# Kernel tuning notes

Hardware: AMD Instinct MI355X
Metric: run time of the kernel (lower is better)

The kernel has to match this reference:

```python
import jax, jax.numpy as jnp
import numpy as np

N_NODES = 50000
N_EDGES = 800000
D = 64
B = 64
HL = 128  # lstm hidden
OUT = 32


def setup_inputs() -> dict:
    key = jax.random.key(0)
    ks = jax.random.split(key, 16)
    s = 0.05
    return {
        "x": jax.random.normal(ks[0], (N_NODES, D), jnp.float32),
        "edge_index": jax.random.randint(ks[1], (2, N_EDGES), 0, N_NODES),
        "batch": jnp.sort(jax.random.randint(ks[2], (N_NODES,), 0, B)),
        "w1": jax.random.normal(ks[3], (D, D), jnp.float32) * s,
        "b1": jnp.zeros((D,), jnp.float32),
        "w2": jax.random.normal(ks[4], (D, D), jnp.float32) * s,
        "b2": jnp.zeros((D,), jnp.float32),
        "w3": jax.random.normal(ks[5], (D, D), jnp.float32) * s,
        "b3": jnp.zeros((D,), jnp.float32),
        "w4": jax.random.normal(ks[6], (D, D), jnp.float32) * s,
        "b4": jnp.zeros((D,), jnp.float32),
        "w_ih": jax.random.normal(ks[7], (4 * HL, D), jnp.float32) * s,
        "w_hh": jax.random.normal(ks[8], (4 * HL, HL), jnp.float32) * s,
        "b_ih": jnp.zeros((4 * HL,), jnp.float32),
        "b_hh": jnp.zeros((4 * HL,), jnp.float32),
        "fc_w": jax.random.normal(ks[9], (OUT, HL), jnp.float32) * s,
        "fc_b": jnp.zeros((OUT,), jnp.float32),
        "h0": jax.random.normal(ks[10], (1, B, HL), jnp.float32),
        "c0": jax.random.normal(ks[11], (1, B, HL), jnp.float32),
    }


def _gin(x, edge_index, wA, bA, wB, bB):
    # GINConv with eps=0: MLP(x + sum_{j->i} x_j); scatter-add over edges
    agg = jax.ops.segment_sum(x[edge_index[0]], edge_index[1], num_segments=N_NODES)
    h = x + agg
    h = jax.nn.relu(h @ wA.T + bA)
    return h @ wB.T + bB


def reference(x, edge_index, batch, w1, b1, w2, b2, w3, b3, w4, b4,
              w_ih, w_hh, b_ih, b_hh, fc_w, fc_b, h0, c0):
    h = jax.nn.relu(_gin(x, edge_index, w1, b1, w2, b2))  # dropout = identity (eval)
    h = jax.nn.relu(_gin(h, edge_index, w3, b3, w4, b4))
    # global_mean_pool over graphs
    sums = jax.ops.segment_sum(h, batch, num_segments=B)              # [B, D]
    cnts = jax.ops.segment_sum(jnp.ones((N_NODES,), h.dtype), batch, num_segments=B)
    pooled = sums / jnp.maximum(cnts, 1.0)[:, None]
    # single-step LSTM (PyTorch gate order: i, f, g, o)
    gates = pooled @ w_ih.T + b_ih + h0[0] @ w_hh.T + b_hh            # [B, 4H]
    i, f, g, o = jnp.split(gates, 4, axis=-1)
    c1 = jax.nn.sigmoid(f) * c0[0] + jax.nn.sigmoid(i) * jnp.tanh(g)
    h1 = jax.nn.sigmoid(o) * jnp.tanh(c1)
    logits = h1 @ fc_w.T + fc_b
    probs = jax.nn.softmax(logits, axis=1)
    return probs, h1[None], c1[None]
```

## Files before the change

kernel.cpp:

```cpp
#include <hip/hip_runtime.h>
#include <hip/hip_bf16.h>

#define N_NODES 50000
#define N_EDGES 800000
#define D 64
#define B 64
#define HL 128
#define OUT 32

#define CAP 64
#define STP 72
#define PK 8
#define ZROW N_NODES

#define BINS 196
#define EPB 2048
#define LCAP 48
#define BCAP 4608

typedef __attribute__((ext_vector_type(8))) short          short8;
typedef __attribute__((ext_vector_type(8))) unsigned short ushort8_t;
typedef __attribute__((ext_vector_type(4))) float          floatx4;

__device__ __forceinline__ unsigned short f2bf(float f)
{
    unsigned u = __float_as_uint(f);
    u = (u + 0x7FFFu + ((u >> 16) & 1u)) >> 16;
    return (unsigned short)u;
}
__device__ __forceinline__ float bf2f(unsigned short s)
{
    return __uint_as_float(((unsigned)s) << 16);
}

__global__ __launch_bounds__(256) void cvt_kernel(
    const float* __restrict__ x, unsigned short* __restrict__ xb,
    const float* __restrict__ w1, const float* __restrict__ w2,
    const float* __restrict__ w3, const float* __restrict__ w4,
    unsigned short* __restrict__ wb,
    int* __restrict__ bincnt,
    unsigned short* __restrict__ g, unsigned short* __restrict__ h1)
{
    int i = blockIdx.x * 256 + threadIdx.x;
    const float4 v = reinterpret_cast<const float4*>(x)[i];
    ushort4 o;
    o.x = f2bf(v.x); o.y = f2bf(v.y); o.z = f2bf(v.z); o.w = f2bf(v.w);
    reinterpret_cast<ushort4*>(xb)[i] = o;

    if (blockIdx.x < 64) {
        int j = blockIdx.x * 256 + threadIdx.x;
        int m = j >> 12, off = j & 4095;
        const float* src = (m == 0) ? w1 : (m == 1) ? w2 : (m == 2) ? w3 : w4;
        wb[j] = f2bf(src[off]);
    }

    if (blockIdx.x == 64) {
        int t = threadIdx.x;
        bincnt[t] = 0;
        if (t < D) {
            xb[(size_t)ZROW * D + t] = 0;
            g [(size_t)ZROW * D + t] = 0;
            h1[(size_t)ZROW * D + t] = 0;
        }
    }
}

__global__ __launch_bounds__(256) void binA_kernel(
    const int* __restrict__ ei, int* __restrict__ bincnt,
    unsigned* __restrict__ binbuf)
{
    __shared__ int      lcnt[BINS];
    __shared__ int      gbase[BINS];
    __shared__ unsigned lbuf[BINS * LCAP];

    int t = threadIdx.x;
    if (t < BINS) lcnt[t] = 0;
    __syncthreads();

    int base = blockIdx.x * EPB;
#pragma unroll
    for (int i = 0; i < EPB / 256; ++i) {
        int e = base + i * 256 + t;
        if (e < N_EDGES) {
            int s = ei[e];
            int d = ei[N_EDGES + e];
            int bin = d >> 8;
            unsigned pk = (unsigned)s | ((unsigned)(d & 255) << 16);
            int p = atomicAdd(&lcnt[bin], 1);
            if (p < LCAP) {
                lbuf[bin * LCAP + p] = pk;
            } else {
                int q = atomicAdd(&bincnt[bin], 1);
                if (q < BCAP) binbuf[bin * BCAP + q] = pk;
            }
        }
    }
    __syncthreads();

    if (t < BINS) {
        int m = lcnt[t]; m = (m < LCAP) ? m : LCAP;
        gbase[t] = (m > 0) ? atomicAdd(&bincnt[t], m) : 0;
    }
    __syncthreads();

    int wv = t >> 6, lane = t & 63;
    for (int b = wv; b < BINS; b += 4) {
        int m = lcnt[b]; m = (m < LCAP) ? m : LCAP;
        int gb = gbase[b];
        for (int j = lane; j < m; j += 64)
            if (gb + j < BCAP) binbuf[b * BCAP + gb + j] = lbuf[b * LCAP + j];
    }
}

__global__ __launch_bounds__(256) void binB_kernel(
    const int*      __restrict__ bincnt,
    const unsigned* __restrict__ binbuf,
    int*            __restrict__ cnt,
    unsigned short* __restrict__ bucket)
{
    __shared__ int            lc[256];
    __shared__ unsigned short lbkt[256 * CAP];

    int t = threadIdx.x;
    lc[t] = 0;
    {
        ushort8_t fill = {ZROW, ZROW, ZROW, ZROW, ZROW, ZROW, ZROW, ZROW};
        for (int idx = t; idx < 256 * CAP / 8; idx += 256)
            reinterpret_cast<ushort8_t*>(lbkt)[idx] = fill;
    }
    __syncthreads();

    int bin = blockIdx.x;
    int m = bincnt[bin]; m = (m < BCAP) ? m : BCAP;
    const unsigned* src = binbuf + bin * BCAP;
    for (int j = t; j < m; j += 256) {
        unsigned pk = src[j];
        int dlow = (pk >> 16) & 255;
        int p = atomicAdd(&lc[dlow], 1);
        if (p < CAP) lbkt[dlow * CAP + p] = (unsigned short)(pk & 0xFFFFu);
    }
    __syncthreads();

    int n0 = bin * 256;
    int n = n0 + t;
    if (n < N_NODES) cnt[n] = (lc[t] < CAP) ? lc[t] : CAP;

    for (int idx = t; idx < 256 * 8; idx += 256) {
        int r = idx >> 3, c = idx & 7;
        if (n0 + r < N_NODES)
            *reinterpret_cast<ushort8_t*>(
                bucket + (size_t)(n0 + r) * CAP + c * 8) =
                *reinterpret_cast<const ushort8_t*>(&lbkt[r * CAP + c * 8]);
    }
}

__global__ __launch_bounds__(256) void gather_kernel(
    const unsigned short* __restrict__ feat,
    const int*            __restrict__ cnt,
    const unsigned short* __restrict__ bucket,
    unsigned short*       __restrict__ outp)
{
    int wv = threadIdx.x >> 6, lane = threadIdx.x & 63;
    int n = blockIdx.x * 4 + wv;

    int deg = cnt[n];
    deg = (deg < CAP) ? deg : CAP;
    int rounds = (deg + 15) >> 4;
    const unsigned short* bkt = bucket + (size_t)n * CAP;

    float acc = bf2f(feat[(size_t)n * D + lane]);
    for (int r = 0; r < rounds; ++r) {
        ushort8_t ia = *reinterpret_cast<const ushort8_t*>(bkt + r * 16);
        ushort8_t ib = *reinterpret_cast<const ushort8_t*>(bkt + r * 16 + 8);
        float v0 = bf2f(feat[(size_t)ia[0] * D + lane]);
        float v1 = bf2f(feat[(size_t)ia[1] * D + lane]);
        float v2 = bf2f(feat[(size_t)ia[2] * D + lane]);
        float v3 = bf2f(feat[(size_t)ia[3] * D + lane]);
        float v4 = bf2f(feat[(size_t)ia[4] * D + lane]);
        float v5 = bf2f(feat[(size_t)ia[5] * D + lane]);
        float v6 = bf2f(feat[(size_t)ia[6] * D + lane]);
        float v7 = bf2f(feat[(size_t)ia[7] * D + lane]);
        float v8 = bf2f(feat[(size_t)ib[0] * D + lane]);
        float v9 = bf2f(feat[(size_t)ib[1] * D + lane]);
        float va = bf2f(feat[(size_t)ib[2] * D + lane]);
        float vb = bf2f(feat[(size_t)ib[3] * D + lane]);
        float vc = bf2f(feat[(size_t)ib[4] * D + lane]);
        float vd = bf2f(feat[(size_t)ib[5] * D + lane]);
        float ve = bf2f(feat[(size_t)ib[6] * D + lane]);
        float vf = bf2f(feat[(size_t)ib[7] * D + lane]);
        acc += (((v0 + v1) + (v2 + v3)) + ((v4 + v5) + (v6 + v7)))
             + (((v8 + v9) + (va + vb)) + ((vc + vd) + (ve + vf)));
    }
    outp[(size_t)n * D + lane] = f2bf(acc);
}

__global__ __launch_bounds__(256) void mlp_kernel(
    const unsigned short* __restrict__ feat,
    const unsigned short* __restrict__ wAb,
    const float*          __restrict__ bA,
    const unsigned short* __restrict__ wBb,
    const float*          __restrict__ bB,
    unsigned short*       __restrict__ outp)
{
    __shared__ __align__(16) unsigned short st[4][16 * STP];

    const int wv   = threadIdx.x >> 6;
    const int lane = threadIdx.x & 63;
    const int quad = lane >> 4;
    const int col  = lane & 15;

    const int n0 = (blockIdx.x * 4 + wv) * 16;
    if (n0 >= N_NODES) return;

    float bAl[4], bBl[4];
#pragma unroll
    for (int t = 0; t < 4; ++t) {
        bAl[t] = bA[t * 16 + col];
        bBl[t] = bB[t * 16 + col];
    }

    short8 WA[4][2], WB[4][2];
#pragma unroll
    for (int t = 0; t < 4; ++t)
#pragma unroll
        for (int k = 0; k < 2; ++k) {
            WA[t][k] = *reinterpret_cast<const short8*>(
                wAb + (t * 16 + col) * D + k * 32 + quad * 8);
            WB[t][k] = *reinterpret_cast<const short8*>(
                wBb + (t * 16 + col) * D + k * 32 + quad * 8);
        }

    short8 A0 = *reinterpret_cast<const short8*>(
        feat + (size_t)(n0 + col) * D + 0 * 32 + quad * 8);
    short8 A1 = *reinterpret_cast<const short8*>(
        feat + (size_t)(n0 + col) * D + 1 * 32 + quad * 8);

    unsigned short* stw = &st[wv][0];

#pragma unroll
    for (int t = 0; t < 4; ++t) {
        floatx4 c = {0.0f, 0.0f, 0.0f, 0.0f};
        c = __builtin_amdgcn_mfma_f32_16x16x32_bf16(A0, WA[t][0], c, 0, 0, 0);
        c = __builtin_amdgcn_mfma_f32_16x16x32_bf16(A1, WA[t][1], c, 0, 0, 0);
#pragma unroll
        for (int r = 0; r < 4; ++r) {
            float v = fmaxf(c[r] + bAl[t], 0.0f);
            stw[(quad * 4 + r) * STP + t * 16 + col] = f2bf(v);
        }
    }

    short8 T0 = *reinterpret_cast<const short8*>(stw + col * STP + 0 * 32 + quad * 8);
    short8 T1 = *reinterpret_cast<const short8*>(stw + col * STP + 1 * 32 + quad * 8);

#pragma unroll
    for (int t = 0; t < 4; ++t) {
        floatx4 c = {0.0f, 0.0f, 0.0f, 0.0f};
        c = __builtin_amdgcn_mfma_f32_16x16x32_bf16(T0, WB[t][0], c, 0, 0, 0);
        c = __builtin_amdgcn_mfma_f32_16x16x32_bf16(T1, WB[t][1], c, 0, 0, 0);
#pragma unroll
        for (int r = 0; r < 4; ++r) {
            float v = fmaxf(c[r] + bBl[t], 0.0f);
            outp[(size_t)(n0 + quad * 4 + r) * D + t * 16 + col] = f2bf(v);
        }
    }
}

__device__ __forceinline__ int lower_bound_dev(const int* a, int n, int v)
{
    int lo = 0, hi = n;
    while (lo < hi) {
        int m = (lo + hi) >> 1;
        if (a[m] < v) lo = m + 1; else hi = m;
    }
    return lo;
}

__global__ __launch_bounds__(256) void pool_partial_kernel(
    const unsigned short* __restrict__ feat,
    const int*            __restrict__ batch,
    float*                __restrict__ psum)
{
    int b = blockIdx.x >> 3;
    int k = blockIdx.x & (PK - 1);
    int start = lower_bound_dev(batch, N_NODES, b);
    int end   = lower_bound_dev(batch, N_NODES, b + 1);

    int d = threadIdx.x & 63;
    int r = threadIdx.x >> 6;

    float acc = 0.0f;
    for (int n = start + k * 4 + r; n < end; n += PK * 4)
        acc += bf2f(feat[(size_t)n * D + d]);

    __shared__ float red[4][D];
    red[r][d] = acc;
    __syncthreads();
    if (r == 0)
        psum[((size_t)b * PK + k) * D + d] =
            red[0][d] + red[1][d] + red[2][d] + red[3][d];
}

__device__ __forceinline__ float sigmoidf_(float x) { return 1.0f / (1.0f + expf(-x)); }

__global__ __launch_bounds__(512) void head_kernel(
    const float* __restrict__ psum,
    const int*   __restrict__ batch,
    const float* __restrict__ w_ih,
    const float* __restrict__ w_hh,
    const float* __restrict__ b_ih,
    const float* __restrict__ b_hh,
    const float* __restrict__ fc_w,
    const float* __restrict__ fc_b,
    const float* __restrict__ h0,
    const float* __restrict__ c0,
    float*       __restrict__ out_probs,
    float*       __restrict__ out_h1,
    float*       __restrict__ out_c1)
{
    int b = blockIdx.x;
    int j = threadIdx.x;

    __shared__ float sp[D];
    __shared__ float sh[HL];
    __shared__ float gates[4 * HL];
    __shared__ float sh1[HL];
    __shared__ float slog[OUT];

    if (j < D) {
        int start = lower_bound_dev(batch, N_NODES, b);
        int end   = lower_bound_dev(batch, N_NODES, b + 1);
        float s = 0.0f;
#pragma unroll
        for (int k = 0; k < PK; ++k) s += psum[((size_t)b * PK + k) * D + j];
        sp[j] = s / fmaxf((float)(end - start), 1.0f);
    } else if (j < D + HL) {
        sh[j - D] = h0[b * HL + (j - D)];
    }
    __syncthreads();

    {
        float acc = b_ih[j] + b_hh[j];
#pragma unroll
        for (int k = 0; k < D; ++k)  acc = fmaf(sp[k], w_ih[j * D + k], acc);
#pragma unroll
        for (int k = 0; k < HL; ++k) acc = fmaf(sh[k], w_hh[j * HL + k], acc);
        gates[j] = acc;
    }
    __syncthreads();

    if (j < HL) {
        float ig = gates[j];
        float fg = gates[HL + j];
        float gg = gates[2 * HL + j];
        float og = gates[3 * HL + j];
        float c  = sigmoidf_(fg) * c0[b * HL + j] + sigmoidf_(ig) * tanhf(gg);
        float hv = sigmoidf_(og) * tanhf(c);
        out_c1[b * HL + j] = c;
        out_h1[b * HL + j] = hv;
        sh1[j] = hv;
    }
    __syncthreads();

    if (j < OUT) {
        float a = fc_b[j];
#pragma unroll
        for (int k = 0; k < HL; ++k) a = fmaf(sh1[k], fc_w[j * HL + k], a);
        slog[j] = a;
    }
    __syncthreads();

    if (j < OUT) {
        float m = -1e30f;
#pragma unroll
        for (int k = 0; k < OUT; ++k) m = fmaxf(m, slog[k]);
        float s = 0.0f;
#pragma unroll
        for (int k = 0; k < OUT; ++k) s += expf(slog[k] - m);
        out_probs[b * OUT + j] = expf(slog[j] - m) / s;
    }
}

extern "C" void kernel_launch(void* const* d_in, const int* in_sizes, int n_in,
                              void* d_out, int out_size, void* d_ws, size_t ws_size,
                              hipStream_t stream)
{
    const float* x     = (const float*)d_in[0];
    const int*   ei    = (const int*)  d_in[1];
    const int*   batch = (const int*)  d_in[2];
    const float* w1    = (const float*)d_in[3];
    const float* b1    = (const float*)d_in[4];
    const float* w2    = (const float*)d_in[5];
    const float* b2    = (const float*)d_in[6];
    const float* w3    = (const float*)d_in[7];
    const float* b3    = (const float*)d_in[8];
    const float* w4    = (const float*)d_in[9];
    const float* b4    = (const float*)d_in[10];
    const float* w_ih  = (const float*)d_in[11];
    const float* w_hh  = (const float*)d_in[12];
    const float* b_ih  = (const float*)d_in[13];
    const float* b_hh  = (const float*)d_in[14];
    const float* fc_w  = (const float*)d_in[15];
    const float* fc_b  = (const float*)d_in[16];
    const float* h0    = (const float*)d_in[17];
    const float* c0    = (const float*)d_in[18];

    const size_t NR = (size_t)N_NODES + 16;
    int* bincnt = (int*)d_ws;
    int* cnt    = bincnt + 256;
    unsigned* binbuf = (unsigned*)(cnt + N_NODES);
    unsigned short* bucket = (unsigned short*)(binbuf + (size_t)BINS * BCAP);
    unsigned short* xb = bucket + (size_t)N_NODES * CAP;
    unsigned short* g  = xb + NR * D;
    unsigned short* h1 = g  + NR * D;
    unsigned short* wb = h1 + NR * D;
    float* psum = (float*)(wb + 4 * D * D);

    float* out_probs = (float*)d_out;
    float* out_h1    = out_probs + B * OUT;
    float* out_c1    = out_h1 + B * HL;

    const int cb = N_NODES * D / 4 / 256;
    const int ab = (N_EDGES + EPB - 1) / EPB;
    const int gb = N_NODES / 4;
    const int mb = (N_NODES / 16 + 3) / 4;

    cvt_kernel<<<cb, 256, 0, stream>>>(x, xb, w1, w2, w3, w4, wb, bincnt, g, h1);

    binA_kernel<<<ab, 256, 0, stream>>>(ei, bincnt, binbuf);
    binB_kernel<<<BINS, 256, 0, stream>>>(bincnt, binbuf, cnt, bucket);

    gather_kernel<<<gb, 256, 0, stream>>>(xb, cnt, bucket, g);
    mlp_kernel<<<mb, 256, 0, stream>>>(g, wb, b1, wb + 4096, b2, h1);

    gather_kernel<<<gb, 256, 0, stream>>>(h1, cnt, bucket, g);
    mlp_kernel<<<mb, 256, 0, stream>>>(g, wb + 8192, b3, wb + 12288, b4, xb);

    pool_partial_kernel<<<B * PK, 256, 0, stream>>>(xb, batch, psum);
    head_kernel<<<B, 512, 0, stream>>>(psum, batch, w_ih, w_hh, b_ih, b_hh,
                                       fc_w, fc_b, h0, c0,
                                       out_probs, out_h1, out_c1);
}
```

Before: 224.0 us.

## Gather layer-1 directly from fp32 input and process two nodes per wave

Removes the full x-to-bf16 conversion pass; the first gather now reads fp32 x directly, with a clamped index and a zero value standing in for the padding row. Both gathers now handle two destination nodes per wave, interleaving their neighbour loads to raise memory-level parallelism. The cost is twice the bytes per random fp32 row read in layer 1, and wasted loads when the two nodes have unequal degree, since the loop runs to the larger one.

```diff
diff --git a/kernel.cpp b/kernel.cpp
--- a/kernel.cpp
+++ b/kernel.cpp
@@ -33,35 +33,22 @@
     return __uint_as_float(((unsigned)s) << 16);
 }
 
-__global__ __launch_bounds__(256) void cvt_kernel(
-    const float* __restrict__ x, unsigned short* __restrict__ xb,
+__global__ __launch_bounds__(256) void init_kernel(
     const float* __restrict__ w1, const float* __restrict__ w2,
     const float* __restrict__ w3, const float* __restrict__ w4,
     unsigned short* __restrict__ wb,
     int* __restrict__ bincnt,
-    unsigned short* __restrict__ g, unsigned short* __restrict__ h1)
-{
-    int i = blockIdx.x * 256 + threadIdx.x;
-    const float4 v = reinterpret_cast<const float4*>(x)[i];
-    ushort4 o;
-    o.x = f2bf(v.x); o.y = f2bf(v.y); o.z = f2bf(v.z); o.w = f2bf(v.w);
-    reinterpret_cast<ushort4*>(xb)[i] = o;
-
+    unsigned short* __restrict__ h1)
+{
     if (blockIdx.x < 64) {
         int j = blockIdx.x * 256 + threadIdx.x;
         int m = j >> 12, off = j & 4095;
         const float* src = (m == 0) ? w1 : (m == 1) ? w2 : (m == 2) ? w3 : w4;
         wb[j] = f2bf(src[off]);
-    }
-
-    if (blockIdx.x == 64) {
+    } else {
         int t = threadIdx.x;
         bincnt[t] = 0;
-        if (t < D) {
-            xb[(size_t)ZROW * D + t] = 0;
-            g [(size_t)ZROW * D + t] = 0;
-            h1[(size_t)ZROW * D + t] = 0;
-        }
+        if (t < D) h1[(size_t)ZROW * D + t] = 0;
     }
 }
 
@@ -154,44 +141,95 @@
     }
 }
 
-__global__ __launch_bounds__(256) void gather_kernel(
+__device__ __forceinline__ float xload(const float* x, int idx, int lane)
+{
+    int ic = (idx < N_NODES) ? idx : (N_NODES - 1);
+    float v = x[(size_t)ic * D + lane];
+    return (idx < N_NODES) ? v : 0.0f;
+}
+
+__global__ __launch_bounds__(256) void gather1_kernel(
+    const float*          __restrict__ x,
+    const int*            __restrict__ cnt,
+    const unsigned short* __restrict__ bucket,
+    unsigned short*       __restrict__ outp)
+{
+    int wv = threadIdx.x >> 6, lane = threadIdx.x & 63;
+    int na = (blockIdx.x * 4 + wv) * 2;
+    int nb = na + 1;
+
+    int da = cnt[na]; da = (da < CAP) ? da : CAP;
+    int db = cnt[nb]; db = (db < CAP) ? db : CAP;
+    int rmax = ((da > db ? da : db) + 15) >> 4;
+    rmax = (rmax > 1) ? rmax : 1;
+
+    const unsigned short* ba = bucket + (size_t)na * CAP;
+    const unsigned short* bb = bucket + (size_t)nb * CAP;
+
+    float acca = x[(size_t)na * D + lane];
+    float accb = x[(size_t)nb * D + lane];
+
+    for (int r = 0; r < rmax; ++r) {
+        ushort8_t i0 = *reinterpret_cast<const ushort8_t*>(ba + r * 16);
+        ushort8_t i1 = *reinterpret_cast<const ushort8_t*>(ba + r * 16 + 8);
+        ushort8_t j0 = *reinterpret_cast<const ushort8_t*>(bb + r * 16);
+        ushort8_t j1 = *reinterpret_cast<const ushort8_t*>(bb + r * 16 + 8);
+        float sa = 0.0f, sb = 0.0f;
+#pragma unroll
+        for (int k = 0; k < 8; ++k) sa += xload(x, i0[k], lane);
+#pragma unroll
+        for (int k = 0; k < 8; ++k) sa += xload(x, i1[k], lane);
+#pragma unroll
+        for (int k = 0; k < 8; ++k) sb += xload(x, j0[k], lane);
+#pragma unroll
+        for (int k = 0; k < 8; ++k) sb += xload(x, j1[k], lane);
+        acca += sa;
+        accb += sb;
+    }
+    outp[(size_t)na * D + lane] = f2bf(acca);
+    outp[(size_t)nb * D + lane] = f2bf(accb);
+}
+
+__global__ __launch_bounds__(256) void gather2_kernel(
     const unsigned short* __restrict__ feat,
     const int*            __restrict__ cnt,
     const unsigned short* __restrict__ bucket,
     unsigned short*       __restrict__ outp)
 {
     int wv = threadIdx.x >> 6, lane = threadIdx.x & 63;
-    int n = blockIdx.x * 4 + wv;
-
-    int deg = cnt[n];
-    deg = (deg < CAP) ? deg : CAP;
-    int rounds = (deg + 15) >> 4;
-    const unsigned short* bkt = bucket + (size_t)n * CAP;
-
-    float acc = bf2f(feat[(size_t)n * D + lane]);
-    for (int r = 0; r < rounds; ++r) {
-        ushort8_t ia = *reinterpret_cast<const ushort8_t*>(bkt + r * 16);
-        ushort8_t ib = *reinterpret_cast<const ushort8_t*>(bkt + r * 16 + 8);
-        float v0 = bf2f(feat[(size_t)ia[0] * D + lane]);
-        float v1 = bf2f(feat[(size_t)ia[1] * D + lane]);
-        float v2 = bf2f(feat[(size_t)ia[2] * D + lane]);
-        float v3 = bf2f(feat[(size_t)ia[3] * D + lane]);
-        float v4 = bf2f(feat[(size_t)ia[4] * D + lane]);
-        float v5 = bf2f(feat[(size_t)ia[5] * D + lane]);
-        float v6 = bf2f(feat[(size_t)ia[6] * D + lane]);
-        float v7 = bf2f(feat[(size_t)ia[7] * D + lane]);
-        float v8 = bf2f(feat[(size_t)ib[0] * D + lane]);
-        float v9 = bf2f(feat[(size_t)ib[1] * D + lane]);
-        float va = bf2f(feat[(size_t)ib[2] * D + lane]);
-        float vb = bf2f(feat[(size_t)ib[3] * D + lane]);
-        float vc = bf2f(feat[(size_t)ib[4] * D + lane]);
-        float vd = bf2f(feat[(size_t)ib[5] * D + lane]);
-        float ve = bf2f(feat[(size_t)ib[6] * D + lane]);
-        float vf = bf2f(feat[(size_t)ib[7] * D + lane]);
-        acc += (((v0 + v1) + (v2 + v3)) + ((v4 + v5) + (v6 + v7)))
-             + (((v8 + v9) + (va + vb)) + ((vc + vd) + (ve + vf)));
-    }
-    outp[(size_t)n * D + lane] = f2bf(acc);
+    int na = (blockIdx.x * 4 + wv) * 2;
+    int nb = na + 1;
+
+    int da = cnt[na]; da = (da < CAP) ? da : CAP;
+    int db = cnt[nb]; db = (db < CAP) ? db : CAP;
+    int rmax = ((da > db ? da : db) + 15) >> 4;
+    rmax = (rmax > 1) ? rmax : 1;
+
+    const unsigned short* ba = bucket + (size_t)na * CAP;
+    const unsigned short* bb = bucket + (size_t)nb * CAP;
+
+    float acca = bf2f(feat[(size_t)na * D + lane]);
+    float accb = bf2f(feat[(size_t)nb * D + lane]);
+
+    for (int r = 0; r < rmax; ++r) {
+        ushort8_t i0 = *reinterpret_cast<const ushort8_t*>(ba + r * 16);
+        ushort8_t i1 = *reinterpret_cast<const ushort8_t*>(ba + r * 16 + 8);
+        ushort8_t j0 = *reinterpret_cast<const ushort8_t*>(bb + r * 16);
+        ushort8_t j1 = *reinterpret_cast<const ushort8_t*>(bb + r * 16 + 8);
+        float sa = 0.0f, sb = 0.0f;
+#pragma unroll
+        for (int k = 0; k < 8; ++k) sa += bf2f(feat[(size_t)i0[k] * D + lane]);
+#pragma unroll
+        for (int k = 0; k < 8; ++k) sa += bf2f(feat[(size_t)i1[k] * D + lane]);
+#pragma unroll
+        for (int k = 0; k < 8; ++k) sb += bf2f(feat[(size_t)j0[k] * D + lane]);
+#pragma unroll
+        for (int k = 0; k < 8; ++k) sb += bf2f(feat[(size_t)j1[k] * D + lane]);
+        acca += sa;
+        accb += sb;
+    }
+    outp[(size_t)na * D + lane] = f2bf(acca);
+    outp[(size_t)nb * D + lane] = f2bf(accb);
 }
 
 __global__ __launch_bounds__(256) void mlp_kernel(
@@ -409,33 +447,32 @@
     int* cnt    = bincnt + 256;
     unsigned* binbuf = (unsigned*)(cnt + N_NODES);
     unsigned short* bucket = (unsigned short*)(binbuf + (size_t)BINS * BCAP);
-    unsigned short* xb = bucket + (size_t)N_NODES * CAP;
-    unsigned short* g  = xb + NR * D;
+    unsigned short* g  = bucket + (size_t)N_NODES * CAP;
     unsigned short* h1 = g  + NR * D;
-    unsigned short* wb = h1 + NR * D;
+    unsigned short* f2 = h1 + NR * D;
+    unsigned short* wb = f2 + NR * D;
     float* psum = (float*)(wb + 4 * D * D);
 
     float* out_probs = (float*)d_out;
     float* out_h1    = out_probs + B * OUT;
     float* out_c1    = out_h1 + B * HL;
 
-    const int cb = N_NODES * D / 4 / 256;
     const int ab = (N_EDGES + EPB - 1) / EPB;
-    const int gb = N_NODES / 4;
+    const int gb = N_NODES / 8;
     const int mb = (N_NODES / 16 + 3) / 4;
 
-    cvt_kernel<<<cb, 256, 0, stream>>>(x, xb, w1, w2, w3, w4, wb, bincnt, g, h1);
+    init_kernel<<<65, 256, 0, stream>>>(w1, w2, w3, w4, wb, bincnt, h1);
 
     binA_kernel<<<ab, 256, 0, stream>>>(ei, bincnt, binbuf);
     binB_kernel<<<BINS, 256, 0, stream>>>(bincnt, binbuf, cnt, bucket);
 
-    gather_kernel<<<gb, 256, 0, stream>>>(xb, cnt, bucket, g);
+    gather1_kernel<<<gb, 256, 0, stream>>>(x, cnt, bucket, g);
     mlp_kernel<<<mb, 256, 0, stream>>>(g, wb, b1, wb + 4096, b2, h1);
 
-    gather_kernel<<<gb, 256, 0, stream>>>(h1, cnt, bucket, g);
-    mlp_kernel<<<mb, 256, 0, stream>>>(g, wb + 8192, b3, wb + 12288, b4, xb);
-
-    pool_partial_kernel<<<B * PK, 256, 0, stream>>>(xb, batch, psum);
+    gather2_kernel<<<gb, 256, 0, stream>>>(h1, cnt, bucket, g);
+    mlp_kernel<<<mb, 256, 0, stream>>>(g, wb + 8192, b3, wb + 12288, b4, f2);
+
+    pool_partial_kernel<<<B * PK, 256, 0, stream>>>(f2, batch, psum);
     head_kernel<<<B, 512, 0, stream>>>(psum, batch, w_ih, w_hh, b_ih, b_hh,
                                        fc_w, fc_b, h0, c0,
                                        out_probs, out_h1, out_c1);
```

Result: no change. 224.6 us (+0.3%).

## Split neighbor gather into two half-dimension passes for cache locality

Applied to the files above, without the earlier changes.

The gather kernel now handles 32 feature dimensions per pass, with each wave covering two nodes, and is launched twice per layer (dims 0-31, then 32-63). The intent is to halve the working set of gathered feature bytes per pass so random neighbor reads hit L2/MALL more often. Outputs use nontemporal stores, and the final MLP writes to a new buffer instead of overwriting xb. The cost is reading the bucket indices twice and one extra kernel launch per layer, and each lane now reads only 64 bytes per row, which makes the accesses less efficient.

```diff
diff --git a/kernel.cpp b/kernel.cpp
--- a/kernel.cpp
+++ b/kernel.cpp
@@ -39,7 +39,7 @@
     const float* __restrict__ w3, const float* __restrict__ w4,
     unsigned short* __restrict__ wb,
     int* __restrict__ bincnt,
-    unsigned short* __restrict__ g, unsigned short* __restrict__ h1)
+    unsigned short* __restrict__ h1)
 {
     int i = blockIdx.x * 256 + threadIdx.x;
     const float4 v = reinterpret_cast<const float4*>(x)[i];
@@ -53,13 +53,11 @@
         const float* src = (m == 0) ? w1 : (m == 1) ? w2 : (m == 2) ? w3 : w4;
         wb[j] = f2bf(src[off]);
     }
-
     if (blockIdx.x == 64) {
         int t = threadIdx.x;
         bincnt[t] = 0;
         if (t < D) {
             xb[(size_t)ZROW * D + t] = 0;
-            g [(size_t)ZROW * D + t] = 0;
             h1[(size_t)ZROW * D + t] = 0;
         }
     }
@@ -158,40 +156,44 @@
     const unsigned short* __restrict__ feat,
     const int*            __restrict__ cnt,
     const unsigned short* __restrict__ bucket,
-    unsigned short*       __restrict__ outp)
-{
-    int wv = threadIdx.x >> 6, lane = threadIdx.x & 63;
-    int n = blockIdx.x * 4 + wv;
+    unsigned short*       __restrict__ outp,
+    int dimoff)
+{
+    int wv   = threadIdx.x >> 6;
+    int lane = threadIdx.x & 63;
+    int half = lane >> 5;
+    int dim  = (lane & 31) + dimoff;
+    int n    = (blockIdx.x * 4 + wv) * 2 + half;
 
     int deg = cnt[n];
     deg = (deg < CAP) ? deg : CAP;
     int rounds = (deg + 15) >> 4;
     const unsigned short* bkt = bucket + (size_t)n * CAP;
 
-    float acc = bf2f(feat[(size_t)n * D + lane]);
+    float acc = bf2f(feat[(size_t)n * D + dim]);
     for (int r = 0; r < rounds; ++r) {
-        ushort8_t ia = *reinterpret_cast<const ushort8_t*>(bkt + r * 16);
-        ushort8_t ib = *reinterpret_cast<const ushort8_t*>(bkt + r * 16 + 8);
-        float v0 = bf2f(feat[(size_t)ia[0] * D + lane]);
-        float v1 = bf2f(feat[(size_t)ia[1] * D + lane]);
-        float v2 = bf2f(feat[(size_t)ia[2] * D + lane]);
-        float v3 = bf2f(feat[(size_t)ia[3] * D + lane]);
-        float v4 = bf2f(feat[(size_t)ia[4] * D + lane]);
-        float v5 = bf2f(feat[(size_t)ia[5] * D + lane]);
-        float v6 = bf2f(feat[(size_t)ia[6] * D + lane]);
-        float v7 = bf2f(feat[(size_t)ia[7] * D + lane]);
-        float v8 = bf2f(feat[(size_t)ib[0] * D + lane]);
-        float v9 = bf2f(feat[(size_t)ib[1] * D + lane]);
-        float va = bf2f(feat[(size_t)ib[2] * D + lane]);
-        float vb = bf2f(feat[(size_t)ib[3] * D + lane]);
-        float vc = bf2f(feat[(size_t)ib[4] * D + lane]);
-        float vd = bf2f(feat[(size_t)ib[5] * D + lane]);
-        float ve = bf2f(feat[(size_t)ib[6] * D + lane]);
-        float vf = bf2f(feat[(size_t)ib[7] * D + lane]);
+        ushort8_t i0 = *reinterpret_cast<const ushort8_t*>(bkt + r * 16);
+        ushort8_t i1 = *reinterpret_cast<const ushort8_t*>(bkt + r * 16 + 8);
+        float v0 = bf2f(feat[(size_t)i0[0] * D + dim]);
+        float v1 = bf2f(feat[(size_t)i0[1] * D + dim]);
+        float v2 = bf2f(feat[(size_t)i0[2] * D + dim]);
+        float v3 = bf2f(feat[(size_t)i0[3] * D + dim]);
+        float v4 = bf2f(feat[(size_t)i0[4] * D + dim]);
+        float v5 = bf2f(feat[(size_t)i0[5] * D + dim]);
+        float v6 = bf2f(feat[(size_t)i0[6] * D + dim]);
+        float v7 = bf2f(feat[(size_t)i0[7] * D + dim]);
+        float v8 = bf2f(feat[(size_t)i1[0] * D + dim]);
+        float v9 = bf2f(feat[(size_t)i1[1] * D + dim]);
+        float va = bf2f(feat[(size_t)i1[2] * D + dim]);
+        float vb = bf2f(feat[(size_t)i1[3] * D + dim]);
+        float vc = bf2f(feat[(size_t)i1[4] * D + dim]);
+        float vd = bf2f(feat[(size_t)i1[5] * D + dim]);
+        float ve = bf2f(feat[(size_t)i1[6] * D + dim]);
+        float vf = bf2f(feat[(size_t)i1[7] * D + dim]);
         acc += (((v0 + v1) + (v2 + v3)) + ((v4 + v5) + (v6 + v7)))
              + (((v8 + v9) + (va + vb)) + ((vc + vd) + (ve + vf)));
     }
-    outp[(size_t)n * D + lane] = f2bf(acc);
+    __builtin_nontemporal_store(f2bf(acc), &outp[(size_t)n * D + dim]);
 }
 
 __global__ __launch_bounds__(256) void mlp_kernel(
@@ -412,7 +414,8 @@
     unsigned short* xb = bucket + (size_t)N_NODES * CAP;
     unsigned short* g  = xb + NR * D;
     unsigned short* h1 = g  + NR * D;
-    unsigned short* wb = h1 + NR * D;
+    unsigned short* f2 = h1 + NR * D;
+    unsigned short* wb = f2 + NR * D;
     float* psum = (float*)(wb + 4 * D * D);
 
     float* out_probs = (float*)d_out;
@@ -421,21 +424,23 @@
 
     const int cb = N_NODES * D / 4 / 256;
     const int ab = (N_EDGES + EPB - 1) / EPB;
-    const int gb = N_NODES / 4;
+    const int gb = N_NODES / 8;
     const int mb = (N_NODES / 16 + 3) / 4;
 
-    cvt_kernel<<<cb, 256, 0, stream>>>(x, xb, w1, w2, w3, w4, wb, bincnt, g, h1);
+    cvt_kernel<<<cb, 256, 0, stream>>>(x, xb, w1, w2, w3, w4, wb, bincnt, h1);
 
     binA_kernel<<<ab, 256, 0, stream>>>(ei, bincnt, binbuf);
     binB_kernel<<<BINS, 256, 0, stream>>>(bincnt, binbuf, cnt, bucket);
 
-    gather_kernel<<<gb, 256, 0, stream>>>(xb, cnt, bucket, g);
+    gather_kernel<<<gb, 256, 0, stream>>>(xb, cnt, bucket, g, 0);
+    gather_kernel<<<gb, 256, 0, stream>>>(xb, cnt, bucket, g, 32);
     mlp_kernel<<<mb, 256, 0, stream>>>(g, wb, b1, wb + 4096, b2, h1);
 
-    gather_kernel<<<gb, 256, 0, stream>>>(h1, cnt, bucket, g);
-    mlp_kernel<<<mb, 256, 0, stream>>>(g, wb + 8192, b3, wb + 12288, b4, xb);
-
-    pool_partial_kernel<<<B * PK, 256, 0, stream>>>(xb, batch, psum);
+    gather_kernel<<<gb, 256, 0, stream>>>(h1, cnt, bucket, g, 0);
+    gather_kernel<<<gb, 256, 0, stream>>>(h1, cnt, bucket, g, 32);
+    mlp_kernel<<<mb, 256, 0, stream>>>(g, wb + 8192, b3, wb + 12288, b4, f2);
+
+    pool_partial_kernel<<<B * PK, 256, 0, stream>>>(f2, batch, psum);
     head_kernel<<<B, 512, 0, stream>>>(psum, batch, w_ih, w_hh, b_ih, b_hh,
                                        fc_w, fc_b, h0, c0,
                                        out_probs, out_h1, out_c1);
```

After: 231.1 us. 1.03x slower.

## Fuse convert with edge binning and fuse second MLP with mean-pool atomics

Applied to the files above, without the earlier changes.

Merges the bf16 conversion kernel and the first edge-binning pass into one launch, using block-index ranges, with bincnt zeroed by a memset. Fuses global mean-pool summation into the second MLP kernel: each block does a segmented reduction over its 64 rows and atomically adds into per-graph sums. This removes the write and reread of final node features and one launch, at the cost of float atomics, which make the summation order nondeterministic. The g zero-row init is dropped, so correctness relies on the gather kernel not reading that row of g.

```diff
diff --git a/kernel.cpp b/kernel.cpp
--- a/kernel.cpp
+++ b/kernel.cpp
@@ -10,7 +10,6 @@
 
 #define CAP 64
 #define STP 72
-#define PK 8
 #define ZROW N_NODES
 
 #define BINS 196
@@ -18,6 +17,9 @@
 #define LCAP 48
 #define BCAP 4608
 
+#define AB 391
+#define CB 3125
+
 typedef __attribute__((ext_vector_type(8))) short          short8;
 typedef __attribute__((ext_vector_type(8))) unsigned short ushort8_t;
 typedef __attribute__((ext_vector_type(4))) float          floatx4;
@@ -33,82 +35,82 @@
     return __uint_as_float(((unsigned)s) << 16);
 }
 
-__global__ __launch_bounds__(256) void cvt_kernel(
+__global__ __launch_bounds__(256) void fused_pro_kernel(
+    const int*   __restrict__ ei,
+    int*         __restrict__ bincnt,
+    unsigned*    __restrict__ binbuf,
     const float* __restrict__ x, unsigned short* __restrict__ xb,
     const float* __restrict__ w1, const float* __restrict__ w2,
     const float* __restrict__ w3, const float* __restrict__ w4,
     unsigned short* __restrict__ wb,
-    int* __restrict__ bincnt,
-    unsigned short* __restrict__ g, unsigned short* __restrict__ h1)
-{
-    int i = blockIdx.x * 256 + threadIdx.x;
-    const float4 v = reinterpret_cast<const float4*>(x)[i];
-    ushort4 o;
-    o.x = f2bf(v.x); o.y = f2bf(v.y); o.z = f2bf(v.z); o.w = f2bf(v.w);
-    reinterpret_cast<ushort4*>(xb)[i] = o;
-
-    if (blockIdx.x < 64) {
-        int j = blockIdx.x * 256 + threadIdx.x;
-        int m = j >> 12, off = j & 4095;
-        const float* src = (m == 0) ? w1 : (m == 1) ? w2 : (m == 2) ? w3 : w4;
-        wb[j] = f2bf(src[off]);
-    }
-
-    if (blockIdx.x == 64) {
-        int t = threadIdx.x;
-        bincnt[t] = 0;
-        if (t < D) {
-            xb[(size_t)ZROW * D + t] = 0;
-            g [(size_t)ZROW * D + t] = 0;
-            h1[(size_t)ZROW * D + t] = 0;
-        }
-    }
-}
-
-__global__ __launch_bounds__(256) void binA_kernel(
-    const int* __restrict__ ei, int* __restrict__ bincnt,
-    unsigned* __restrict__ binbuf)
+    unsigned short* __restrict__ h1,
+    float*       __restrict__ psum)
 {
     __shared__ int      lcnt[BINS];
     __shared__ int      gbase[BINS];
     __shared__ unsigned lbuf[BINS * LCAP];
 
     int t = threadIdx.x;
-    if (t < BINS) lcnt[t] = 0;
-    __syncthreads();
-
-    int base = blockIdx.x * EPB;
-#pragma unroll
-    for (int i = 0; i < EPB / 256; ++i) {
-        int e = base + i * 256 + t;
-        if (e < N_EDGES) {
-            int s = ei[e];
-            int d = ei[N_EDGES + e];
-            int bin = d >> 8;
-            unsigned pk = (unsigned)s | ((unsigned)(d & 255) << 16);
-            int p = atomicAdd(&lcnt[bin], 1);
-            if (p < LCAP) {
-                lbuf[bin * LCAP + p] = pk;
-            } else {
-                int q = atomicAdd(&bincnt[bin], 1);
-                if (q < BCAP) binbuf[bin * BCAP + q] = pk;
+
+    if (blockIdx.x < AB) {
+        if (t < BINS) lcnt[t] = 0;
+        __syncthreads();
+
+        int base = blockIdx.x * EPB;
+#pragma unroll
+        for (int i = 0; i < EPB / 256; ++i) {
+            int e = base + i * 256 + t;
+            if (e < N_EDGES) {
+                int s = ei[e];
+                int d = ei[N_EDGES + e];
+                int bin = d >> 8;
+                unsigned pk = (unsigned)s | ((unsigned)(d & 255) << 16);
+                int p = atomicAdd(&lcnt[bin], 1);
+                if (p < LCAP) {
+                    lbuf[bin * LCAP + p] = pk;
+                } else {
+                    int q = atomicAdd(&bincnt[bin], 1);
+                    if (q < BCAP) binbuf[bin * BCAP + q] = pk;
+                }
             }
         }
-    }
-    __syncthreads();
-
-    if (t < BINS) {
-        int m = lcnt[t]; m = (m < LCAP) ? m : LCAP;
-        gbase[t] = (m > 0) ? atomicAdd(&bincnt[t], m) : 0;
-    }
-    __syncthreads();
-
-    int wv = t >> 6, lane = t & 63;
-    for (int b = wv; b < BINS; b += 4) {
-        int m = lcnt[b]; m = (m < LCAP) ? m : LCAP;
-        int gb = gbase[b];
-        for (int j = lane; j < m; j += 64)
-            if (gb + j < BCAP) binbuf[b * BCAP + gb + j] = lbuf[b * LCAP + j];
+        __syncthreads();
+
+        if (t < BINS) {
+            int m = lcnt[t]; m = (m < LCAP) ? m : LCAP;
+            gbase[t] = (m > 0) ? atomicAdd(&bincnt[t], m) : 0;
+        }
+        __syncthreads();
+
+        int wv = t >> 6, lane = t & 63;
+        for (int b = wv; b < BINS; b += 4) {
+            int m = lcnt[b]; m = (m < LCAP) ? m : LCAP;
+            int gb = gbase[b];
+            for (int j = lane; j < m; j += 64)
+                if (gb + j < BCAP) binbuf[b * BCAP + gb + j] = lbuf[b * LCAP + j];
+        }
+    } else if (blockIdx.x < AB + CB) {
+        int cb = blockIdx.x - AB;
+        int i = cb * 256 + t;
+        const float4 v = reinterpret_cast<const float4*>(x)[i];
+        ushort4 o;
+        o.x = f2bf(v.x); o.y = f2bf(v.y); o.z = f2bf(v.z); o.w = f2bf(v.w);
+        reinterpret_cast<ushort4*>(xb)[i] = o;
+
+        if (cb < 64) {
+            int j = cb * 256 + t;
+            int m = j >> 12, off = j & 4095;
+            const float* src = (m == 0) ? w1 : (m == 1) ? w2 : (m == 2) ? w3 : w4;
+            wb[j] = f2bf(src[off]);
+        }
+    } else {
+        if (t < D) {
+            xb[(size_t)ZROW * D + t] = 0;
+            h1[(size_t)ZROW * D + t] = 0;
+        }
+#pragma unroll
+        for (int k = 0; k < 16; ++k)
+            psum[t * 16 + k] = 0.0f;
     }
 }
 
@@ -265,6 +267,116 @@
     }
 }
 
+__global__ __launch_bounds__(256) void mlp2_pool_kernel(
+    const unsigned short* __restrict__ feat,
+    const unsigned short* __restrict__ wAb,
+    const float*          __restrict__ bA,
+    const unsigned short* __restrict__ wBb,
+    const float*          __restrict__ bB,
+    const int*            __restrict__ batch,
+    float*                __restrict__ psum)
+{
+    __shared__ __align__(16) unsigned short st[4][16 * STP];
+    __shared__ float pt[64][D + 1];
+    __shared__ int   sbatch[64];
+
+    const int tid  = threadIdx.x;
+    const int wv   = tid >> 6;
+    const int lane = tid & 63;
+    const int quad = lane >> 4;
+    const int col  = lane & 15;
+
+    const int bn0 = blockIdx.x * 64;
+    const int n0  = bn0 + wv * 16;
+    const bool active = (n0 < N_NODES);
+
+    if (tid < 64) {
+        int n = bn0 + tid;
+        sbatch[tid] = (n < N_NODES) ? batch[n] : -1;
+    }
+
+    if (active) {
+        float bAl[4], bBl[4];
+#pragma unroll
+        for (int t = 0; t < 4; ++t) {
+            bAl[t] = bA[t * 16 + col];
+            bBl[t] = bB[t * 16 + col];
+        }
+
+        short8 WA[4][2], WB[4][2];
+#pragma unroll
+        for (int t = 0; t < 4; ++t)
+#pragma unroll
+            for (int k = 0; k < 2; ++k) {
+                WA[t][k] = *reinterpret_cast<const short8*>(
+                    wAb + (t * 16 + col) * D + k * 32 + quad * 8);
+                WB[t][k] = *reinterpret_cast<const short8*>(
+                    wBb + (t * 16 + col) * D + k * 32 + quad * 8);
+            }
+
+        short8 A0 = *reinterpret_cast<const short8*>(
+            feat + (size_t)(n0 + col) * D + 0 * 32 + quad * 8);
+        short8 A1 = *reinterpret_cast<const short8*>(
+            feat + (size_t)(n0 + col) * D + 1 * 32 + quad * 8);
+
+        unsigned short* stw = &st[wv][0];
+
+#pragma unroll
+        for (int t = 0; t < 4; ++t) {
+            floatx4 c = {0.0f, 0.0f, 0.0f, 0.0f};
+            c = __builtin_amdgcn_mfma_f32_16x16x32_bf16(A0, WA[t][0], c, 0, 0, 0);
+            c = __builtin_amdgcn_mfma_f32_16x16x32_bf16(A1, WA[t][1], c, 0, 0, 0);
+#pragma unroll
+            for (int r = 0; r < 4; ++r) {
+                float v = fmaxf(c[r] + bAl[t], 0.0f);
+                stw[(quad * 4 + r) * STP + t * 16 + col] = f2bf(v);
+            }
+        }
+
+        short8 T0 = *reinterpret_cast<const short8*>(stw + col * STP + 0 * 32 + quad * 8);
+        short8 T1 = *reinterpret_cast<const short8*>(stw + col * STP + 1 * 32 + quad * 8);
+
+#pragma unroll
+        for (int t = 0; t < 4; ++t) {
+            floatx4 c = {0.0f, 0.0f, 0.0f, 0.0f};
+            c = __builtin_amdgcn_mfma_f32_16x16x32_bf16(T0, WB[t][0], c, 0, 0, 0);
+            c = __builtin_amdgcn_mfma_f32_16x16x32_bf16(T1, WB[t][1], c, 0, 0, 0);
+#pragma unroll
+            for (int r = 0; r < 4; ++r) {
+                float v = fmaxf(c[r] + bBl[t], 0.0f);
+                pt[wv * 16 + quad * 4 + r][t * 16 + col] = v;
+            }
+        }
+    } else {
+#pragma unroll
+        for (int r = 0; r < 4; ++r)
+            pt[wv * 16 + quad * 4 + r][(lane & 15) * 4 + (lane >> 4)] = 0.0f;
+        for (int c = 0; c < 4; ++c)
+#pragma unroll
+            for (int r = 0; r < 4; ++r)
+                pt[wv * 16 + quad * 4 + r][c * 16 + col] = 0.0f;
+    }
+    __syncthreads();
+
+    int q = tid >> 6;
+    int d = tid & 63;
+    float acc = 0.0f;
+    int curg = sbatch[q * 16];
+#pragma unroll
+    for (int r = 0; r < 16; ++r) {
+        int row = q * 16 + r;
+        int g = sbatch[row];
+        float v = pt[row][d];
+        if (g != curg) {
+            if (curg >= 0) atomicAdd(&psum[curg * D + d], acc);
+            acc = 0.0f;
+            curg = g;
+        }
+        acc += v;
+    }
+    if (curg >= 0) atomicAdd(&psum[curg * D + d], acc);
+}
+
 __device__ __forceinline__ int lower_bound_dev(const int* a, int n, int v)
 {
     int lo = 0, hi = n;
@@ -273,31 +385,6 @@
         if (a[m] < v) lo = m + 1; else hi = m;
     }
     return lo;
-}
-
-__global__ __launch_bounds__(256) void pool_partial_kernel(
-    const unsigned short* __restrict__ feat,
-    const int*            __restrict__ batch,
-    float*                __restrict__ psum)
-{
-    int b = blockIdx.x >> 3;
-    int k = blockIdx.x & (PK - 1);
-    int start = lower_bound_dev(batch, N_NODES, b);
-    int end   = lower_bound_dev(batch, N_NODES, b + 1);
-
-    int d = threadIdx.x & 63;
-    int r = threadIdx.x >> 6;
-
-    float acc = 0.0f;
-    for (int n = start + k * 4 + r; n < end; n += PK * 4)
-        acc += bf2f(feat[(size_t)n * D + d]);
-
-    __shared__ float red[4][D];
-    red[r][d] = acc;
-    __syncthreads();
-    if (r == 0)
-        psum[((size_t)b * PK + k) * D + d] =
-            red[0][d] + red[1][d] + red[2][d] + red[3][d];
 }
 
 __device__ __forceinline__ float sigmoidf_(float x) { return 1.0f / (1.0f + expf(-x)); }
@@ -329,10 +416,7 @@
     if (j < D) {
         int start = lower_bound_dev(batch, N_NODES, b);
         int end   = lower_bound_dev(batch, N_NODES, b + 1);
-        float s = 0.0f;
-#pragma unroll
-        for (int k = 0; k < PK; ++k) s += psum[((size_t)b * PK + k) * D + j];
-        sp[j] = s / fmaxf((float)(end - start), 1.0f);
+        sp[j] = psum[b * D + j] / fmaxf((float)(end - start), 1.0f);
     } else if (j < D + HL) {
         sh[j - D] = h0[b * HL + (j - D)];
     }
@@ -419,23 +503,22 @@
     float* out_h1    = out_probs + B * OUT;
     float* out_c1    = out_h1 + B * HL;
 
-    const int cb = N_NODES * D / 4 / 256;
-    const int ab = (N_EDGES + EPB - 1) / EPB;
     const int gb = N_NODES / 4;
     const int mb = (N_NODES / 16 + 3) / 4;
 
-    cvt_kernel<<<cb, 256, 0, stream>>>(x, xb, w1, w2, w3, w4, wb, bincnt, g, h1);
-
-    binA_kernel<<<ab, 256, 0, stream>>>(ei, bincnt, binbuf);
+    hipMemsetAsync(bincnt, 0, 256 * sizeof(int), stream);
+    fused_pro_kernel<<<AB + CB + 1, 256, 0, stream>>>(
+        ei, bincnt, binbuf, x, xb, w1, w2, w3, w4, wb, h1, psum);
+
     binB_kernel<<<BINS, 256, 0, stream>>>(bincnt, binbuf, cnt, bucket);
 
     gather_kernel<<<gb, 256, 0, stream>>>(xb, cnt, bucket, g);
     mlp_kernel<<<mb, 256, 0, stream>>>(g, wb, b1, wb + 4096, b2, h1);
 
     gather_kernel<<<gb, 256, 0, stream>>>(h1, cnt, bucket, g);
-    mlp_kernel<<<mb, 256, 0, stream>>>(g, wb + 8192, b3, wb + 12288, b4, xb);
-
-    pool_partial_kernel<<<B * PK, 256, 0, stream>>>(xb, batch, psum);
+    mlp2_pool_kernel<<<mb, 256, 0, stream>>>(g, wb + 8192, b3, wb + 12288, b4,
+                                             batch, psum);
+
     head_kernel<<<B, 512, 0, stream>>>(psum, batch, w_ih, w_hh, b_ih, b_hh,
                                        fc_w, fc_b, h0, c0,
                                        out_probs, out_h1, out_c1);
```

After: 209.9 us. -6.3%, faster.
